# Kernel optimization log

Measured on AMD Instinct MI355X. Metric: run time of the kernel, lower is better.

Reference implementation:

```python
import jax, jax.numpy as jnp
import numpy as np

ALPHA = 0.2          # LeakyReLU negative slope
NEG_INF = -9e15      # mask value from the torch source
N, F_IN, F_OUT = 8192, 128, 64


def setup_inputs() -> dict:
    key = jax.random.key(0)
    k1, k2, k3, k4, k5 = jax.random.split(key, 5)
    X = jax.random.normal(k1, (N, F_IN), dtype=jnp.float32)
    A = jax.random.randint(k2, (N, N), 0, 2, dtype=jnp.int32)  # 0/1 adjacency
    W = jax.random.normal(k3, (F_IN, F_OUT), dtype=jnp.float32) * 0.05
    a1 = jax.random.normal(k4, (F_OUT,), dtype=jnp.float32) * 0.05
    a2 = jax.random.normal(k5, (F_OUT,), dtype=jnp.float32) * 0.05
    return {"X": X, "A": A, "W": W, "a1": a1, "a2": a2}


def reference(X, A, W, a1, a2):
    # h = W(X)  (Linear, no bias)
    h = X @ W                                   # (N, F_out)
    # a([h_i || h_j]) == h_i @ a1 + h_j @ a2  (split of the 2F attention vector)
    s1 = h @ a1                                 # (N,)
    s2 = h @ a2                                 # (N,)
    e = jax.nn.leaky_relu(s1[:, None] + s2[None, :], ALPHA)  # (N, N)
    att = jnp.where(A > 0, e, NEG_INF)
    att = jax.nn.softmax(att, axis=1)           # row-wise masked softmax
    # dropout p=0.0 -> identity
    return att @ h                              # (N, F_out)
```

## Files before the change

kernel.cpp:

```cpp
#include <hip/hip_runtime.h>
#include <hip/hip_bf16.h>

#define NV 8192
#define FIN 128
#define FOUT 64

typedef __attribute__((ext_vector_type(8))) short short8;
typedef __attribute__((ext_vector_type(4))) float floatx4;

__device__ __forceinline__ uint f2bf_u(float f) {
  uint u = __float_as_uint(f);
  return (u + 0x7FFFu + ((u >> 16) & 1u)) >> 16;
}
__device__ __forceinline__ float bf2f(ushort b) {
  return __uint_as_float(((uint)b) << 16);
}

__global__ void k0_detect(const uint* __restrict__ X, int* __restrict__ flag) {
  const int lane = threadIdx.x & 63;
  uint u = X[lane];
  uint e = (u >> 7) & 0xFF;
  bool ok = (e >= 100u) && (e <= 135u);
  unsigned long long b = __ballot(ok);
  if (lane == 0) *flag = (__builtin_popcountll(b) >= 48) ? 1 : 0;
}

__global__ __launch_bounds__(256) void k1_proj(
    const void* __restrict__ Xv, const void* __restrict__ Wv,
    const void* __restrict__ a1v_, const void* __restrict__ a2v_,
    ushort* __restrict__ HtT, float* __restrict__ s1, float* __restrict__ s2,
    const int* __restrict__ flagp)
{
  const int is_bf16 = *flagp;
  const int wave = threadIdx.x >> 6;
  const int lane = threadIdx.x & 63;
  const int i0 = blockIdx.x * 64 + wave * 16;
  const int col = lane & 15;
  const int q   = lane >> 4;

  short8 bfrag[4][4];
  float a1f[4], a2f[4];
  if (is_bf16) {
    const ushort* W = (const ushort*)Wv;
#pragma unroll
    for (int nt = 0; nt < 4; ++nt)
#pragma unroll
      for (int kc = 0; kc < 4; ++kc) {
        short8 b;
#pragma unroll
        for (int j = 0; j < 8; ++j)
          b[j] = (short)W[(kc*32 + q*8 + j)*FOUT + nt*16 + col];
        bfrag[nt][kc] = b;
      }
#pragma unroll
    for (int nt = 0; nt < 4; ++nt) {
      a1f[nt] = bf2f(((const ushort*)a1v_)[nt*16 + col]);
      a2f[nt] = bf2f(((const ushort*)a2v_)[nt*16 + col]);
    }
  } else {
    const float* W = (const float*)Wv;
#pragma unroll
    for (int nt = 0; nt < 4; ++nt)
#pragma unroll
      for (int kc = 0; kc < 4; ++kc) {
        short8 b;
#pragma unroll
        for (int j = 0; j < 8; ++j)
          b[j] = (short)f2bf_u(W[(kc*32 + q*8 + j)*FOUT + nt*16 + col]);
        bfrag[nt][kc] = b;
      }
#pragma unroll
    for (int nt = 0; nt < 4; ++nt) {
      a1f[nt] = ((const float*)a1v_)[nt*16 + col];
      a2f[nt] = ((const float*)a2v_)[nt*16 + col];
    }
  }

  floatx4 acc[4] = {{0.f,0.f,0.f,0.f},{0.f,0.f,0.f,0.f},
                    {0.f,0.f,0.f,0.f},{0.f,0.f,0.f,0.f}};
#pragma unroll
  for (int kc = 0; kc < 4; ++kc) {
    short8 a;
    if (is_bf16) {
      a = *(const short8*)&((const ushort*)Xv)[(size_t)(i0 + col)*FIN + kc*32 + q*8];
    } else {
      const float* X = (const float*)Xv;
      float4 x0 = *(const float4*)&X[(size_t)(i0 + col)*FIN + kc*32 + q*8];
      float4 x1 = *(const float4*)&X[(size_t)(i0 + col)*FIN + kc*32 + q*8 + 4];
      a[0] = (short)f2bf_u(x0.x); a[1] = (short)f2bf_u(x0.y);
      a[2] = (short)f2bf_u(x0.z); a[3] = (short)f2bf_u(x0.w);
      a[4] = (short)f2bf_u(x1.x); a[5] = (short)f2bf_u(x1.y);
      a[6] = (short)f2bf_u(x1.z); a[7] = (short)f2bf_u(x1.w);
    }
#pragma unroll
    for (int nt = 0; nt < 4; ++nt)
      acc[nt] = __builtin_amdgcn_mfma_f32_16x16x32_bf16(a, bfrag[nt][kc], acc[nt], 0, 0, 0);
  }

  float s1p[4] = {0,0,0,0}, s2p[4] = {0,0,0,0};
#pragma unroll
  for (int nt = 0; nt < 4; ++nt) {
    ushort4 pk;
    pk.x = (ushort)f2bf_u(acc[nt][0]);
    pk.y = (ushort)f2bf_u(acc[nt][1]);
    pk.z = (ushort)f2bf_u(acc[nt][2]);
    pk.w = (ushort)f2bf_u(acc[nt][3]);
    *(ushort4*)&HtT[(size_t)(nt*16 + col)*NV + i0 + q*4] = pk;
#pragma unroll
    for (int reg = 0; reg < 4; ++reg) {
      s1p[reg] += acc[nt][reg] * a1f[nt];
      s2p[reg] += acc[nt][reg] * a2f[nt];
    }
  }
#pragma unroll
  for (int m = 1; m < 16; m <<= 1)
#pragma unroll
    for (int reg = 0; reg < 4; ++reg) {
      s1p[reg] += __shfl_xor(s1p[reg], m, 64);
      s2p[reg] += __shfl_xor(s2p[reg], m, 64);
    }
  if (col == 0)
#pragma unroll
    for (int reg = 0; reg < 4; ++reg) {
      s1[i0 + q*4 + reg] = s1p[reg];
      s2[i0 + q*4 + reg] = s2p[reg];
    }
}

#define CT 128
#define NT (NV / CT)
#define PST 136

__global__ __launch_bounds__(256, 6) void k2_attn(
    const int* __restrict__ A, const ushort* __restrict__ HtT,
    const float* __restrict__ s1g, const float* __restrict__ s2g,
    void* __restrict__ outv, const int* __restrict__ flagp)
{
  __shared__ __align__(16) ushort Pl[16 * PST];
  __shared__ __align__(16) ushort Hl[64 * PST];
  __shared__ float Lrow[16];

  const int is_bf16 = *flagp;
  const int tid  = threadIdx.x;
  const int wave = tid >> 6;
  const int lane = tid & 63;
  const int i0   = blockIdx.x * 16;
  const int q    = lane >> 4;
  const int mcol = lane & 15;
  const int r    = tid >> 4;
  const int cb   = (tid & 15) * 8;

  const float s1r = s1g[i0 + r];
  const size_t abase = (size_t)(i0 + r) * NV + cb;

  float Lp = 0.f;
  floatx4 acc = {0.f, 0.f, 0.f, 0.f};

  int4 av0 = *(const int4*)&A[abase];
  int4 av1 = *(const int4*)&A[abase + 4];
  float4 sv0 = *(const float4*)&s2g[cb];
  float4 sv1 = *(const float4*)&s2g[cb + 4];
  short8 hv[4];
#pragma unroll
  for (int it = 0; it < 4; ++it)
    hv[it] = *(const short8*)&HtT[(size_t)(r + 16*it) * NV + cb];

  for (int t = 0; t < NT; ++t) {
    __syncthreads();

    {
      float x0 = s1r + sv0.x, x1 = s1r + sv0.y, x2 = s1r + sv0.z, x3 = s1r + sv0.w;
      float x4 = s1r + sv1.x, x5 = s1r + sv1.y, x6 = s1r + sv1.z, x7 = s1r + sv1.w;
      float w0 = av0.x ? __expf(fmaxf(x0, 0.2f*x0)) : 0.f;
      float w1 = av0.y ? __expf(fmaxf(x1, 0.2f*x1)) : 0.f;
      float w2 = av0.z ? __expf(fmaxf(x2, 0.2f*x2)) : 0.f;
      float w3 = av0.w ? __expf(fmaxf(x3, 0.2f*x3)) : 0.f;
      float w4 = av1.x ? __expf(fmaxf(x4, 0.2f*x4)) : 0.f;
      float w5 = av1.y ? __expf(fmaxf(x5, 0.2f*x5)) : 0.f;
      float w6 = av1.z ? __expf(fmaxf(x6, 0.2f*x6)) : 0.f;
      float w7 = av1.w ? __expf(fmaxf(x7, 0.2f*x7)) : 0.f;
      Lp += ((w0 + w1) + (w2 + w3)) + ((w4 + w5) + (w6 + w7));
      uint4 pk;
      pk.x = f2bf_u(w0) | (f2bf_u(w1) << 16);
      pk.y = f2bf_u(w2) | (f2bf_u(w3) << 16);
      pk.z = f2bf_u(w4) | (f2bf_u(w5) << 16);
      pk.w = f2bf_u(w6) | (f2bf_u(w7) << 16);
      *(uint4*)&Pl[r * PST + cb] = pk;
#pragma unroll
      for (int it = 0; it < 4; ++it)
        *(short8*)&Hl[(r + 16*it) * PST + cb] = hv[it];
    }

    __syncthreads();

    if (t + 1 < NT) {
      const int c = (t + 1) * CT;
      av0 = *(const int4*)&A[abase + c];
      av1 = *(const int4*)&A[abase + c + 4];
      sv0 = *(const float4*)&s2g[c + cb];
      sv1 = *(const float4*)&s2g[c + cb + 4];
#pragma unroll
      for (int it = 0; it < 4; ++it)
        hv[it] = *(const short8*)&HtT[(size_t)(r + 16*it) * NV + c + cb];
    }

#pragma unroll
    for (int kc = 0; kc < 4; ++kc) {
      short8 af = *(const short8*)&Pl[mcol * PST + kc*32 + q*8];
      short8 bf = *(const short8*)&Hl[(wave*16 + mcol) * PST + kc*32 + q*8];
      acc = __builtin_amdgcn_mfma_f32_16x16x32_bf16(af, bf, acc, 0, 0, 0);
    }
  }

#pragma unroll
  for (int m = 1; m < 16; m <<= 1) Lp += __shfl_xor(Lp, m, 64);
  if (mcol == 0) Lrow[r] = Lp;
  __syncthreads();

#pragma unroll
  for (int reg = 0; reg < 4; ++reg) {
    int rr = q*4 + reg;
    float v = acc[reg] / Lrow[rr];
    if (is_bf16)
      ((ushort*)outv)[(size_t)(i0 + rr)*FOUT + wave*16 + mcol] = (ushort)f2bf_u(v);
    else
      ((float*)outv)[(size_t)(i0 + rr)*FOUT + wave*16 + mcol] = v;
  }
}

extern "C" void kernel_launch(void* const* d_in, const int* in_sizes, int n_in,
                              void* d_out, int out_size, void* d_ws, size_t ws_size,
                              hipStream_t stream) {
  const void* X  = d_in[0];
  const int*  A  = (const int*)d_in[1];
  const void* W  = d_in[2];
  const void* a1 = d_in[3];
  const void* a2 = d_in[4];

  char* ws = (char*)d_ws;
  ushort* HtT  = (ushort*)ws;
  float*  s1   = (float*)(ws + (size_t)FOUT*NV*2);
  float*  s2   = s1 + NV;
  int*    flag = (int*)(s2 + NV);

  hipLaunchKernelGGL(k0_detect, dim3(1), dim3(64), 0, stream,
                     (const uint*)X, flag);
  hipLaunchKernelGGL(k1_proj, dim3(NV/64), dim3(256), 0, stream,
                     X, W, a1, a2, HtT, s1, s2, flag);
  hipLaunchKernelGGL(k2_attn, dim3(NV/16), dim3(256), 0, stream,
                     A, HtT, s1, s2, d_out, flag);
}
```

Before: 380.6 us.

## Split attention columns into slices with a separate combine kernel

Splits each row block's column range into four slices run by separate blocks, writing unnormalized partial outputs and row sums to workspace. A new combine kernel sums the partials and normalizes. Each block also starts at a rotated tile offset so blocks do not all read the same HtT/s2 region at once. The aim is more blocks, for better occupancy and a shorter tail, at the cost of extra partial-buffer traffic and one more launch.

```diff
diff --git a/kernel.cpp b/kernel.cpp
--- a/kernel.cpp
+++ b/kernel.cpp
@@ -128,42 +128,51 @@
 }
 
 #define CT 128
-#define NT (NV / CT)
+#define SLICES 4
+#define SW (NV / SLICES)
+#define NT (SW / CT)
 #define PST 136
 
 __global__ __launch_bounds__(256, 6) void k2_attn(
     const int* __restrict__ A, const ushort* __restrict__ HtT,
     const float* __restrict__ s1g, const float* __restrict__ s2g,
-    void* __restrict__ outv, const int* __restrict__ flagp)
+    float* __restrict__ Part, float* __restrict__ Lpart)
 {
   __shared__ __align__(16) ushort Pl[16 * PST];
   __shared__ __align__(16) ushort Hl[64 * PST];
-  __shared__ float Lrow[16];
-
-  const int is_bf16 = *flagp;
+
   const int tid  = threadIdx.x;
   const int wave = tid >> 6;
   const int lane = tid & 63;
-  const int i0   = blockIdx.x * 16;
+  const int sl   = blockIdx.x & (SLICES - 1);
+  const int rb   = blockIdx.x >> 2;
+  const int i0   = rb * 16;
   const int q    = lane >> 4;
   const int mcol = lane & 15;
   const int r    = tid >> 4;
   const int cb   = (tid & 15) * 8;
+  const int c0s  = sl * SW;
+  const int t0   = (rb * 7) & (NT - 1);
 
   const float s1r = s1g[i0 + r];
-  const size_t abase = (size_t)(i0 + r) * NV + cb;
+  const size_t abase = (size_t)(i0 + r) * NV + c0s + cb;
 
   float Lp = 0.f;
   floatx4 acc = {0.f, 0.f, 0.f, 0.f};
 
-  int4 av0 = *(const int4*)&A[abase];
-  int4 av1 = *(const int4*)&A[abase + 4];
-  float4 sv0 = *(const float4*)&s2g[cb];
-  float4 sv1 = *(const float4*)&s2g[cb + 4];
+  int4 av0, av1;
+  float4 sv0, sv1;
   short8 hv[4];
-#pragma unroll
-  for (int it = 0; it < 4; ++it)
-    hv[it] = *(const short8*)&HtT[(size_t)(r + 16*it) * NV + cb];
+  {
+    const int c = t0 * CT;
+    av0 = *(const int4*)&A[abase + c];
+    av1 = *(const int4*)&A[abase + c + 4];
+    sv0 = *(const float4*)&s2g[c0s + c + cb];
+    sv1 = *(const float4*)&s2g[c0s + c + cb + 4];
+#pragma unroll
+    for (int it = 0; it < 4; ++it)
+      hv[it] = *(const short8*)&HtT[(size_t)(r + 16*it) * NV + c0s + c + cb];
+  }
 
   for (int t = 0; t < NT; ++t) {
     __syncthreads();
@@ -194,14 +203,14 @@
     __syncthreads();
 
     if (t + 1 < NT) {
-      const int c = (t + 1) * CT;
-      av0 = *(const int4*)&A[abase + c];
-      av1 = *(const int4*)&A[abase + c + 4];
-      sv0 = *(const float4*)&s2g[c + cb];
-      sv1 = *(const float4*)&s2g[c + cb + 4];
+      const int c2 = ((t + 1 + t0) & (NT - 1)) * CT;
+      av0 = *(const int4*)&A[abase + c2];
+      av1 = *(const int4*)&A[abase + c2 + 4];
+      sv0 = *(const float4*)&s2g[c0s + c2 + cb];
+      sv1 = *(const float4*)&s2g[c0s + c2 + cb + 4];
 #pragma unroll
       for (int it = 0; it < 4; ++it)
-        hv[it] = *(const short8*)&HtT[(size_t)(r + 16*it) * NV + c + cb];
+        hv[it] = *(const short8*)&HtT[(size_t)(r + 16*it) * NV + c0s + c2 + cb];
     }
 
 #pragma unroll
@@ -214,17 +223,41 @@
 
 #pragma unroll
   for (int m = 1; m < 16; m <<= 1) Lp += __shfl_xor(Lp, m, 64);
-  if (mcol == 0) Lrow[r] = Lp;
-  __syncthreads();
+  if (mcol == 0) Lpart[(size_t)sl * NV + i0 + r] = Lp;
 
 #pragma unroll
   for (int reg = 0; reg < 4; ++reg) {
     int rr = q*4 + reg;
-    float v = acc[reg] / Lrow[rr];
-    if (is_bf16)
-      ((ushort*)outv)[(size_t)(i0 + rr)*FOUT + wave*16 + mcol] = (ushort)f2bf_u(v);
-    else
-      ((float*)outv)[(size_t)(i0 + rr)*FOUT + wave*16 + mcol] = v;
+    Part[((size_t)sl * NV + i0 + rr) * FOUT + wave*16 + mcol] = acc[reg];
+  }
+}
+
+__global__ __launch_bounds__(256) void k3_combine(
+    const float* __restrict__ Part, const float* __restrict__ Lpart,
+    void* __restrict__ outv, const int* __restrict__ flagp)
+{
+  const int is_bf16 = *flagp;
+  const int g   = blockIdx.x * 256 + threadIdx.x;
+  const int row = g >> 4;
+  const int fb  = (g & 15) * 4;
+
+  float4 s = {0.f, 0.f, 0.f, 0.f};
+  float L = 0.f;
+#pragma unroll
+  for (int sl = 0; sl < SLICES; ++sl) {
+    float4 v = *(const float4*)&Part[((size_t)sl * NV + row) * FOUT + fb];
+    s.x += v.x; s.y += v.y; s.z += v.z; s.w += v.w;
+    L += Lpart[(size_t)sl * NV + row];
+  }
+  const float inv = __frcp_rn(L);
+  s.x *= inv; s.y *= inv; s.z *= inv; s.w *= inv;
+  if (is_bf16) {
+    ushort4 pk;
+    pk.x = (ushort)f2bf_u(s.x); pk.y = (ushort)f2bf_u(s.y);
+    pk.z = (ushort)f2bf_u(s.z); pk.w = (ushort)f2bf_u(s.w);
+    *(ushort4*)&((ushort*)outv)[(size_t)row * FOUT + fb] = pk;
+  } else {
+    *(float4*)&((float*)outv)[(size_t)row * FOUT + fb] = s;
   }
 }
 
@@ -238,15 +271,19 @@
   const void* a2 = d_in[4];
 
   char* ws = (char*)d_ws;
-  ushort* HtT  = (ushort*)ws;
-  float*  s1   = (float*)(ws + (size_t)FOUT*NV*2);
-  float*  s2   = s1 + NV;
-  int*    flag = (int*)(s2 + NV);
+  ushort* HtT   = (ushort*)ws;
+  float*  s1    = (float*)(ws + (size_t)FOUT*NV*2);
+  float*  s2    = s1 + NV;
+  int*    flag  = (int*)(s2 + NV);
+  float*  Part  = (float*)((char*)flag + 16);
+  float*  Lpart = Part + (size_t)SLICES * NV * FOUT;
 
   hipLaunchKernelGGL(k0_detect, dim3(1), dim3(64), 0, stream,
                      (const uint*)X, flag);
   hipLaunchKernelGGL(k1_proj, dim3(NV/64), dim3(256), 0, stream,
                      X, W, a1, a2, HtT, s1, s2, flag);
-  hipLaunchKernelGGL(k2_attn, dim3(NV/16), dim3(256), 0, stream,
-                     A, HtT, s1, s2, d_out, flag);
-}
+  hipLaunchKernelGGL(k2_attn, dim3((NV/16) * SLICES), dim3(256), 0, stream,
+                     A, HtT, s1, s2, Part, Lpart);
+  hipLaunchKernelGGL(k3_combine, dim3(NV*FOUT/4/256), dim3(256), 0, stream,
+                     Part, Lpart, d_out, flag);
+}
```

Measured after the change: 381.0 us. Within noise of the previous version (+0.1%).
